# Optimization experiments

Measured on AMD Instinct MI355X. Metric: run time of the kernel, lower is better.

The kernel has to match this reference:

```python
import jax, jax.numpy as jnp
import numpy as np

B, T, C, H = 2, 2048, 1024, 16
HD = C // H
MAX_WAVELENGTH = 10000.0


def apply_rope(x, positions):
    # x: [B, H, T, HD], positions: [T]
    fraction = 2.0 * jnp.arange(HD // 2, dtype=jnp.float32) / HD
    timescale = MAX_WAVELENGTH ** fraction  # [HD//2]
    sinusoid = positions[:, None] / timescale[None, :]  # [T, HD//2]
    sin = jnp.sin(sinusoid)
    cos = jnp.cos(sinusoid)
    first, second = jnp.split(x, 2, axis=-1)
    out = jnp.concatenate(
        [first * cos - second * sin, second * cos + first * sin], axis=-1
    )
    return out.astype(x.dtype)


def setup_inputs() -> dict:
    key = jax.random.key(0)
    k1, k2, k3 = jax.random.split(key, 3)
    x = jax.random.normal(k1, (B, T, C), dtype=jnp.float32)
    w_attn = jax.random.normal(k2, (C, 3 * C), dtype=jnp.float32) * 0.02
    b_attn = jnp.zeros((3 * C,), dtype=jnp.float32)
    w_proj = jax.random.normal(k3, (C, C), dtype=jnp.float32) * 0.02
    b_proj = jnp.zeros((C,), dtype=jnp.float32)
    return {"x": x, "w_attn": w_attn, "b_attn": b_attn,
            "w_proj": w_proj, "b_proj": b_proj}


def reference(x, w_attn, b_attn, w_proj, b_proj):
    b, t, c = x.shape
    qkv = x @ w_attn + b_attn  # [B, T, 3C]
    q, k, v = jnp.split(qkv, 3, axis=-1)
    q = q.reshape(b, t, H, HD).transpose(0, 2, 1, 3)  # [B, H, T, HD]
    k = k.reshape(b, t, H, HD).transpose(0, 2, 1, 3)
    v = v.reshape(b, t, H, HD).transpose(0, 2, 1, 3)
    positions = jnp.arange(t, dtype=x.dtype)
    q = apply_rope(q, positions)
    k = apply_rope(k, positions)
    att = jnp.einsum('bhqd,bhkd->bhqk', q, k) * (1.0 / jnp.sqrt(HD))
    causal = jnp.tril(jnp.ones((t, t), dtype=bool))
    att = jnp.where(causal, att, jnp.finfo(att.dtype).min)
    att = jax.nn.softmax(att, axis=-1)
    y = jnp.einsum('bhqk,bhkd->bhqd', att, v)
    y = y.transpose(0, 2, 1, 3).reshape(b, t, c)
    return y @ w_proj + b_proj
```

## Files before the change

### kernel.cpp

```cpp
#include <hip/hip_runtime.h>
#include <hip/hip_bf16.h>


typedef __attribute__((ext_vector_type(8))) short short8;
typedef __attribute__((ext_vector_type(4))) float floatx4;

__device__ __forceinline__ unsigned short f2bf(float f) {
    union { float f; unsigned int u; } v; v.f = f;
    unsigned int r = v.u + 0x7FFFu + ((v.u >> 16) & 1u);
    return (unsigned short)(r >> 16);
}

__device__ __forceinline__ unsigned int pk2bf(float a, float b) {
    union { float f; unsigned int u; } ua, ub;
    ua.f = a; ub.f = b;
    return __builtin_amdgcn_perm(ub.u + 0x8000u, ua.u + 0x8000u, 0x07060302u);
}

__device__ __forceinline__ void gld16(const void* g, void* l) {
    __builtin_amdgcn_global_load_lds(
        (const __attribute__((address_space(1))) unsigned int*)g,
        (__attribute__((address_space(3))) unsigned int*)l, 16, 0, 0);
}

__device__ __forceinline__ void transpose_body(
    const float* __restrict__ in, unsigned short* __restrict__ out,
    int R, int NC, int bx, int by, int tid,
    unsigned short (*tile)[65]) {
    int r0 = by * 64, c0 = bx * 64;
    int col = tid & 63, rr = tid >> 6;
#pragma unroll
    for (int i = 0; i < 16; i++) {
        int row = rr + i * 4;
        tile[row][col] = f2bf(in[(size_t)(r0 + row) * NC + c0 + col]);
    }
    __syncthreads();
#pragma unroll
    for (int i = 0; i < 16; i++) {
        int orow = rr + i * 4;
        out[(size_t)(c0 + orow) * R + r0 + col] = tile[col][orow];
    }
}

__global__ __launch_bounds__(256) void prep(
    const float* __restrict__ x,
    const float* __restrict__ w_attn,
    const float* __restrict__ w_proj,
    unsigned short* __restrict__ x_bf,
    unsigned short* __restrict__ wTa,
    unsigned short* __restrict__ wTp,
    float2* __restrict__ tab) {
    __shared__ unsigned short tile[64][65];
    int bid = blockIdx.x;
    int tid = threadIdx.x;
    if (bid < 4096) {
        int i = bid * 256 + tid;
        float4 v = ((const float4*)x)[i];
        ushort4 o;
        o.x = f2bf(v.x); o.y = f2bf(v.y); o.z = f2bf(v.z); o.w = f2bf(v.w);
        ((ushort4*)x_bf)[i] = o;
    } else if (bid < 4864) {
        int t = bid - 4096;
        transpose_body(w_attn, wTa, 1024, 3072, t % 48, t / 48, tid, tile);
    } else if (bid < 5120) {
        int t = bid - 4864;
        transpose_body(w_proj, wTp, 1024, 1024, t & 15, t >> 4, tid, tile);
    } else {
        int i = (bid - 5120) * 256 + tid;
        int t = i >> 5, d = i & 31;
        float inv_ts = exp2f(-0.41524101186092036f * (float)d);
        float ang = (float)t * inv_ts;
        tab[i] = make_float2(sinf(ang), cosf(ang));
    }
}

__global__ __launch_bounds__(256) void gemm_qkv(
    const unsigned short* __restrict__ A,
    const unsigned short* __restrict__ BT,
    const float* __restrict__ bias,
    const float2* __restrict__ tab,
    unsigned short* __restrict__ qT,
    unsigned short* __restrict__ kT,
    unsigned short* __restrict__ vT) {
    __shared__ __align__(16) unsigned short smem[16384];
    unsigned short* as = smem;
    unsigned short* bs = smem + 8192;
    int tid = threadIdx.x;
    int lane = tid & 63;
    int w = tid >> 6;
    int wx = w & 1, wy = w >> 1;
    int l16 = lane & 15, quad = lane >> 4;
    int m0 = blockIdx.y * 128;
    int n0 = blockIdx.x * 128;
    int x = l16 & 7;
    int lr = lane >> 3;
    int gc = (lane & 7) ^ lr;

    floatx4 acc[4][4];
#pragma unroll
    for (int mi = 0; mi < 4; mi++)
#pragma unroll
        for (int ni = 0; ni < 4; ni++)
            acc[mi][ni] = (floatx4){0.f, 0.f, 0.f, 0.f};

    for (int k0 = 0; k0 < 1024; k0 += 64) {
        __syncthreads();
#pragma unroll
        for (int i = 0; i < 4; i++) {
            int seg = w * 4 + i;
            int row = seg * 8 + lr;
            gld16(A + (size_t)(m0 + row) * 1024 + k0 + gc * 8, &as[seg * 512]);
            gld16(BT + (size_t)(n0 + row) * 1024 + k0 + gc * 8, &bs[seg * 512]);
        }
        __syncthreads();
#pragma unroll
        for (int kk = 0; kk < 2; kk++) {
            short8 af[4], bf[4];
#pragma unroll
            for (int mi = 0; mi < 4; mi++) {
                int r = wy * 64 + mi * 16 + l16;
                af[mi] = *(const short8*)&as[r * 64 + (((kk << 2) | quad) ^ x) * 8];
            }
#pragma unroll
            for (int ni = 0; ni < 4; ni++) {
                int r = wx * 64 + ni * 16 + l16;
                bf[ni] = *(const short8*)&bs[r * 64 + (((kk << 2) | quad) ^ x) * 8];
            }
#pragma unroll
            for (int mi = 0; mi < 4; mi++)
#pragma unroll
                for (int ni = 0; ni < 4; ni++)
                    acc[mi][ni] = __builtin_amdgcn_mfma_f32_16x16x32_bf16(
                        af[mi], bf[ni], acc[mi][ni], 0, 0, 0);
        }
    }

    int region = n0 >> 10;
    int b = m0 >> 11;
    float b0 = bias[n0 + wx * 64 + l16];
    float b1 = bias[n0 + wx * 64 + 16 + l16];
    float b2 = bias[n0 + wx * 64 + 32 + l16];
    float b3 = bias[n0 + wx * 64 + 48 + l16];

    if (region < 2) {
        unsigned short* qk = region ? kT : qT;
        float scale = region ? 1.0f : 0.125f;
        int h = ((n0 & 1023) + wx * 64) >> 6;
        unsigned short* obase = qk + (size_t)(b * 16 + h) * 2048 * 64;
#pragma unroll
        for (int mi = 0; mi < 4; mi++)
#pragma unroll
            for (int r = 0; r < 4; r++) {
                int t = (m0 & 2047) + wy * 64 + mi * 16 + quad * 4 + r;
                float2 sc0 = tab[t * 32 + l16];
                float2 sc1 = tab[t * 32 + 16 + l16];
                float v1 = acc[mi][0][r] + b0, v2 = acc[mi][2][r] + b2;
                float w1 = acc[mi][1][r] + b1, w2 = acc[mi][3][r] + b3;
                unsigned short* orow = obase + (size_t)t * 64;
                orow[l16]      = f2bf((v1 * sc0.y - v2 * sc0.x) * scale);
                orow[l16 + 32] = f2bf((v2 * sc0.y + v1 * sc0.x) * scale);
                orow[l16 + 16] = f2bf((w1 * sc1.y - w2 * sc1.x) * scale);
                orow[l16 + 48] = f2bf((w2 * sc1.y + w1 * sc1.x) * scale);
            }
    } else {
        __syncthreads();
#pragma unroll
        for (int mi = 0; mi < 4; mi++)
#pragma unroll
            for (int ni = 0; ni < 4; ni++) {
                int d_loc = wx * 64 + ni * 16 + l16;
                int t_base = wy * 64 + mi * 16 + quad * 4;
                float bv = (ni == 0) ? b0 : (ni == 1) ? b1 : (ni == 2) ? b2 : b3;
                uint2 pk;
                pk.x = pk2bf(acc[mi][ni][0] + bv, acc[mi][ni][1] + bv);
                pk.y = pk2bf(acc[mi][ni][2] + bv, acc[mi][ni][3] + bv);
                int e = d_loc * 128 + (t_base ^ ((d_loc & 15) << 3));
                *(uint2*)&smem[e] = pk;
            }
        __syncthreads();
        int d_r = tid >> 1, half = tid & 1;
        int cv = (n0 - 2048) + d_r;
        int hh = cv >> 6, dd = cv & 63;
        int fofs = (d_r & 15) << 3;
        size_t vbase = ((size_t)(b * 16 + hh) * 64 + dd) * 2048 + (m0 & 2047);
#pragma unroll
        for (int c = 0; c < 8; c++) {
            int tc = half * 64 + c * 8;
            short8 val = *(const short8*)&smem[d_r * 128 + (tc ^ fofs)];
            *(short8*)&vT[vbase + tc] = val;
        }
    }
}

__global__ __launch_bounds__(256) void gemm_proj(
    const unsigned short* __restrict__ A,
    const unsigned short* __restrict__ BT,
    const float* __restrict__ bias,
    float* __restrict__ out) {
    __shared__ __align__(16) unsigned short as[128 * 64];
    __shared__ __align__(16) unsigned short bs[64 * 64];
    int lane = threadIdx.x & 63;
    int w = threadIdx.x >> 6;
    int wx = w & 1, wy = w >> 1;
    int l16 = lane & 15, quad = lane >> 4;
    int m0 = blockIdx.y * 128;
    int n0 = blockIdx.x * 64;
    int x = l16 & 7;
    int lr = lane >> 3;
    int gc = (lane & 7) ^ lr;

    floatx4 acc[4][2];
#pragma unroll
    for (int mi = 0; mi < 4; mi++)
#pragma unroll
        for (int ni = 0; ni < 2; ni++)
            acc[mi][ni] = (floatx4){0.f, 0.f, 0.f, 0.f};

    for (int k0 = 0; k0 < 1024; k0 += 64) {
        __syncthreads();
#pragma unroll
        for (int i = 0; i < 6; i++) {
            int seg = w * 6 + i;
            if (seg < 16) {
                int row = seg * 8 + lr;
                gld16(A + (size_t)(m0 + row) * 1024 + k0 + gc * 8, &as[seg * 512]);
            } else {
                int s2 = seg - 16;
                int row = s2 * 8 + lr;
                gld16(BT + (size_t)(n0 + row) * 1024 + k0 + gc * 8, &bs[s2 * 512]);
            }
        }
        __syncthreads();
#pragma unroll
        for (int kk = 0; kk < 2; kk++) {
            short8 af[4], bf[2];
#pragma unroll
            for (int mi = 0; mi < 4; mi++) {
                int r = wy * 64 + mi * 16 + l16;
                af[mi] = *(const short8*)&as[r * 64 + (((kk << 2) | quad) ^ x) * 8];
            }
#pragma unroll
            for (int ni = 0; ni < 2; ni++) {
                int r = wx * 32 + ni * 16 + l16;
                bf[ni] = *(const short8*)&bs[r * 64 + (((kk << 2) | quad) ^ x) * 8];
            }
#pragma unroll
            for (int mi = 0; mi < 4; mi++)
#pragma unroll
                for (int ni = 0; ni < 2; ni++)
                    acc[mi][ni] = __builtin_amdgcn_mfma_f32_16x16x32_bf16(
                        af[mi], bf[ni], acc[mi][ni], 0, 0, 0);
        }
    }

#pragma unroll
    for (int mi = 0; mi < 4; mi++)
#pragma unroll
        for (int ni = 0; ni < 2; ni++) {
            int row = m0 + wy * 64 + mi * 16 + quad * 4;
            int col = n0 + wx * 32 + ni * 16 + l16;
            float bv = bias[col];
#pragma unroll
            for (int r = 0; r < 4; r++)
                out[(size_t)(row + r) * 1024 + col] = acc[mi][ni][r] + bv;
        }
}

__global__ __launch_bounds__(512) void attn4(
    const unsigned short* __restrict__ qT,
    const unsigned short* __restrict__ kT,
    const unsigned short* __restrict__ vT,
    unsigned short* __restrict__ y) {
    __shared__ __align__(16) unsigned short kbuf[2][64 * 64];
    __shared__ __align__(16) unsigned short vbuf[2][64 * 64];
    __shared__ __align__(16) unsigned short pl[8][16 * 88];
    int lane = threadIdx.x & 63;
    int w = threadIdx.x >> 6;
    int l16 = lane & 15, quad = lane >> 4;
    int blk = blockIdx.x;
    int idx = blk >> 5;
    int qb = (idx < 8) ? (15 - idx * 2) : ((idx - 8) * 2);
    int bh = blk & 31;
    int b = bh >> 4, h = bh & 15;
    int q0 = qb * 128 + w * 16;
    int dt = 2 * qb + (w >> 2);
    const unsigned short* qp = qT + (size_t)bh * 2048 * 64;
    const unsigned short* kp = kT + (size_t)bh * 2048 * 64;
    const unsigned short* vp = vT + (size_t)bh * 64 * 2048;
    unsigned short* plw = pl[w];
    int x = l16 & 7;

    short8 qf0 = *(const short8*)(qp + (size_t)(q0 + l16) * 64 + quad * 8);
    short8 qf1 = *(const short8*)(qp + (size_t)(q0 + l16) * 64 + 32 + quad * 8);

    floatx4 acc[4];
#pragma unroll
    for (int ni = 0; ni < 4; ni++) acc[ni] = (floatx4){0.f, 0.f, 0.f, 0.f};
    float l_part = 0.f;

    auto stage = [&](int bi, int j0) {
#pragma unroll
        for (int i = 0; i < 2; i++) {
            int t = w * 2 + i;
            if (t < 8) {
                int r = t * 8 + (lane >> 3);
                int c = (lane & 7) ^ (r & 7);
                gld16(kp + (size_t)(j0 + r) * 64 + c * 8, &kbuf[bi][t * 512]);
            } else {
                int s = t - 8;
                int d = s * 8 + (lane >> 3);
                int c = (lane & 7) ^ (d & 7);
                gld16(vp + (size_t)d * 2048 + j0 + c * 8, &vbuf[bi][s * 512]);
            }
        }
    };

    int L = 2 * qb + 2;
    stage(0, 0);
    for (int it = 0; it < L; it++) {
        int j0 = it * 64;
        int bi = it & 1;
        __syncthreads();
        if (it + 1 < L) stage(bi ^ 1, j0 + 64);
        if (it > dt) continue;
        const unsigned short* kb = kbuf[bi];
        const unsigned short* vb = vbuf[bi];
        bool diag = (it == dt);
        floatx4 s[4];
#pragma unroll
        for (int c = 0; c < 4; c++) {
            int r = c * 16 + l16;
            short8 kf0 = *(const short8*)&kb[r * 64 + ((quad) ^ x) * 8];
            short8 kf1 = *(const short8*)&kb[r * 64 + ((quad | 4) ^ x) * 8];
            floatx4 z = (floatx4){0.f, 0.f, 0.f, 0.f};
            z = __builtin_amdgcn_mfma_f32_16x16x32_bf16(kf0, qf0, z, 0, 0, 0);
            z = __builtin_amdgcn_mfma_f32_16x16x32_bf16(kf1, qf1, z, 0, 0, 0);
            s[c] = z;
        }
        int query = q0 + l16;
#pragma unroll
        for (int c = 0; c < 4; c++) {
            float p[4];
#pragma unroll
            for (int r = 0; r < 4; r++) {
                float e = __expf(s[c][r]);
                if (diag) {
                    int key = j0 + c * 16 + quad * 4 + r;
                    e = (key <= query) ? e : 0.f;
                }
                p[r] = e;
            }
            l_part += (p[0] + p[1]) + (p[2] + p[3]);
            uint2 pk = {pk2bf(p[0], p[1]), pk2bf(p[2], p[3])};
            *(uint2*)&plw[l16 * 88 + c * 16 + quad * 4] = pk;
        }
        short8 pa0 = *(const short8*)&plw[l16 * 88 + quad * 8];
        short8 pa1 = *(const short8*)&plw[l16 * 88 + 32 + quad * 8];
#pragma unroll
        for (int ni = 0; ni < 4; ni++) {
            int d = ni * 16 + l16;
            short8 vf0 = *(const short8*)&vb[d * 64 + ((quad) ^ x) * 8];
            short8 vf1 = *(const short8*)&vb[d * 64 + ((quad | 4) ^ x) * 8];
            acc[ni] = __builtin_amdgcn_mfma_f32_16x16x32_bf16(pa0, vf0, acc[ni], 0, 0, 0);
            acc[ni] = __builtin_amdgcn_mfma_f32_16x16x32_bf16(pa1, vf1, acc[ni], 0, 0, 0);
        }
    }

    float tot = l_part;
    tot += __shfl_xor(tot, 16, 64);
    tot += __shfl_xor(tot, 32, 64);
    float inv[4];
#pragma unroll
    for (int r = 0; r < 4; r++)
        inv[r] = 1.f / __shfl(tot, quad * 4 + r, 16);
#pragma unroll
    for (int ni = 0; ni < 4; ni++)
#pragma unroll
        for (int r = 0; r < 4; r++) {
            int t = q0 + quad * 4 + r;
            y[((size_t)(b * 2048 + t)) * 1024 + h * 64 + ni * 16 + l16] =
                f2bf(acc[ni][r] * inv[r]);
        }
}

extern "C" void kernel_launch(void* const* d_in, const int* in_sizes, int n_in,
                              void* d_out, int out_size, void* d_ws, size_t ws_size,
                              hipStream_t stream) {
    const float* x      = (const float*)d_in[0];
    const float* w_attn = (const float*)d_in[1];
    const float* b_attn = (const float*)d_in[2];
    const float* w_proj = (const float*)d_in[3];
    const float* b_proj = (const float*)d_in[4];
    float* out = (float*)d_out;

    char* ws = (char*)d_ws;
    unsigned short* x_bf = (unsigned short*)ws;
    unsigned short* wTa  = (unsigned short*)(ws + (8ull << 20));
    unsigned short* wTp  = (unsigned short*)(ws + (14ull << 20));
    unsigned short* qTb  = (unsigned short*)(ws + (16ull << 20));
    unsigned short* kTb  = (unsigned short*)(ws + (24ull << 20));
    unsigned short* vTb  = (unsigned short*)(ws + (32ull << 20));
    float2*         tab  = (float2*)(ws + (40ull << 20));
    unsigned short* y_bf = x_bf;

    prep<<<5376, 256, 0, stream>>>(x, w_attn, w_proj, x_bf, wTa, wTp, tab);
    gemm_qkv<<<dim3(24, 32), 256, 0, stream>>>(x_bf, wTa, b_attn, tab,
                                               qTb, kTb, vTb);
    attn4<<<512, 512, 0, stream>>>(qTb, kTb, vTb, y_bf);
    gemm_proj<<<dim3(16, 32), 256, 0, stream>>>(y_bf, wTp, b_proj, out);
}
```

Measured before the change: 182.7 us.

## Give each attention wave two 16-row query tiles to reuse K/V fragments

The attention kernel now runs 4 waves per block instead of 8, and each wave handles 32 query rows as two 16-row tiles. Each K and V fragment read from LDS feeds two MFMAs, which halves LDS fragment traffic per query. Each wave now also stages four K/V chunks instead of two. The cost is higher register use from doubled accumulators, and fewer waves available to hide latency.

```diff
diff --git a/kernel.cpp b/kernel.cpp
--- a/kernel.cpp
+++ b/kernel.cpp
@@ -266,14 +266,14 @@
         }
 }
 
-__global__ __launch_bounds__(512) void attn4(
+__global__ __launch_bounds__(256) void attn5(
     const unsigned short* __restrict__ qT,
     const unsigned short* __restrict__ kT,
     const unsigned short* __restrict__ vT,
     unsigned short* __restrict__ y) {
     __shared__ __align__(16) unsigned short kbuf[2][64 * 64];
     __shared__ __align__(16) unsigned short vbuf[2][64 * 64];
-    __shared__ __align__(16) unsigned short pl[8][16 * 88];
+    __shared__ __align__(16) unsigned short pl[4][32 * 88];
     int lane = threadIdx.x & 63;
     int w = threadIdx.x >> 6;
     int l16 = lane & 15, quad = lane >> 4;
@@ -282,26 +282,31 @@
     int qb = (idx < 8) ? (15 - idx * 2) : ((idx - 8) * 2);
     int bh = blk & 31;
     int b = bh >> 4, h = bh & 15;
-    int q0 = qb * 128 + w * 16;
-    int dt = 2 * qb + (w >> 2);
+    int q0 = qb * 128 + w * 32;
+    int dt = 2 * qb + (w >> 1);
     const unsigned short* qp = qT + (size_t)bh * 2048 * 64;
     const unsigned short* kp = kT + (size_t)bh * 2048 * 64;
     const unsigned short* vp = vT + (size_t)bh * 64 * 2048;
     unsigned short* plw = pl[w];
     int x = l16 & 7;
 
-    short8 qf0 = *(const short8*)(qp + (size_t)(q0 + l16) * 64 + quad * 8);
-    short8 qf1 = *(const short8*)(qp + (size_t)(q0 + l16) * 64 + 32 + quad * 8);
-
-    floatx4 acc[4];
-#pragma unroll
-    for (int ni = 0; ni < 4; ni++) acc[ni] = (floatx4){0.f, 0.f, 0.f, 0.f};
-    float l_part = 0.f;
+    short8 qA0 = *(const short8*)(qp + (size_t)(q0 + l16) * 64 + quad * 8);
+    short8 qA1 = *(const short8*)(qp + (size_t)(q0 + l16) * 64 + 32 + quad * 8);
+    short8 qB0 = *(const short8*)(qp + (size_t)(q0 + 16 + l16) * 64 + quad * 8);
+    short8 qB1 = *(const short8*)(qp + (size_t)(q0 + 16 + l16) * 64 + 32 + quad * 8);
+
+    floatx4 accA[4], accB[4];
+#pragma unroll
+    for (int ni = 0; ni < 4; ni++) {
+        accA[ni] = (floatx4){0.f, 0.f, 0.f, 0.f};
+        accB[ni] = (floatx4){0.f, 0.f, 0.f, 0.f};
+    }
+    float lpA = 0.f, lpB = 0.f;
 
     auto stage = [&](int bi, int j0) {
 #pragma unroll
-        for (int i = 0; i < 2; i++) {
-            int t = w * 2 + i;
+        for (int i = 0; i < 4; i++) {
+            int t = w * 4 + i;
             if (t < 8) {
                 int r = t * 8 + (lane >> 3);
                 int c = (lane & 7) ^ (r & 7);
@@ -326,60 +331,74 @@
         const unsigned short* kb = kbuf[bi];
         const unsigned short* vb = vbuf[bi];
         bool diag = (it == dt);
-        floatx4 s[4];
+        int queryA = q0 + l16, queryB = q0 + 16 + l16;
 #pragma unroll
         for (int c = 0; c < 4; c++) {
             int r = c * 16 + l16;
             short8 kf0 = *(const short8*)&kb[r * 64 + ((quad) ^ x) * 8];
             short8 kf1 = *(const short8*)&kb[r * 64 + ((quad | 4) ^ x) * 8];
-            floatx4 z = (floatx4){0.f, 0.f, 0.f, 0.f};
-            z = __builtin_amdgcn_mfma_f32_16x16x32_bf16(kf0, qf0, z, 0, 0, 0);
-            z = __builtin_amdgcn_mfma_f32_16x16x32_bf16(kf1, qf1, z, 0, 0, 0);
-            s[c] = z;
-        }
-        int query = q0 + l16;
-#pragma unroll
-        for (int c = 0; c < 4; c++) {
-            float p[4];
-#pragma unroll
-            for (int r = 0; r < 4; r++) {
-                float e = __expf(s[c][r]);
+            floatx4 zA = (floatx4){0.f, 0.f, 0.f, 0.f};
+            zA = __builtin_amdgcn_mfma_f32_16x16x32_bf16(kf0, qA0, zA, 0, 0, 0);
+            zA = __builtin_amdgcn_mfma_f32_16x16x32_bf16(kf1, qA1, zA, 0, 0, 0);
+            floatx4 zB = (floatx4){0.f, 0.f, 0.f, 0.f};
+            zB = __builtin_amdgcn_mfma_f32_16x16x32_bf16(kf0, qB0, zB, 0, 0, 0);
+            zB = __builtin_amdgcn_mfma_f32_16x16x32_bf16(kf1, qB1, zB, 0, 0, 0);
+            float pA[4], pB[4];
+#pragma unroll
+            for (int rr = 0; rr < 4; rr++) {
+                float eA = __expf(zA[rr]);
+                float eB = __expf(zB[rr]);
                 if (diag) {
-                    int key = j0 + c * 16 + quad * 4 + r;
-                    e = (key <= query) ? e : 0.f;
+                    int key = j0 + c * 16 + quad * 4 + rr;
+                    eA = (key <= queryA) ? eA : 0.f;
+                    eB = (key <= queryB) ? eB : 0.f;
                 }
-                p[r] = e;
-            }
-            l_part += (p[0] + p[1]) + (p[2] + p[3]);
-            uint2 pk = {pk2bf(p[0], p[1]), pk2bf(p[2], p[3])};
-            *(uint2*)&plw[l16 * 88 + c * 16 + quad * 4] = pk;
-        }
-        short8 pa0 = *(const short8*)&plw[l16 * 88 + quad * 8];
-        short8 pa1 = *(const short8*)&plw[l16 * 88 + 32 + quad * 8];
+                pA[rr] = eA; pB[rr] = eB;
+            }
+            lpA += (pA[0] + pA[1]) + (pA[2] + pA[3]);
+            lpB += (pB[0] + pB[1]) + (pB[2] + pB[3]);
+            uint2 ka = {pk2bf(pA[0], pA[1]), pk2bf(pA[2], pA[3])};
+            uint2 kbv = {pk2bf(pB[0], pB[1]), pk2bf(pB[2], pB[3])};
+            *(uint2*)&plw[l16 * 88 + c * 16 + quad * 4] = ka;
+            *(uint2*)&plw[(16 + l16) * 88 + c * 16 + quad * 4] = kbv;
+        }
+        short8 paA0 = *(const short8*)&plw[l16 * 88 + quad * 8];
+        short8 paA1 = *(const short8*)&plw[l16 * 88 + 32 + quad * 8];
+        short8 paB0 = *(const short8*)&plw[(16 + l16) * 88 + quad * 8];
+        short8 paB1 = *(const short8*)&plw[(16 + l16) * 88 + 32 + quad * 8];
 #pragma unroll
         for (int ni = 0; ni < 4; ni++) {
             int d = ni * 16 + l16;
             short8 vf0 = *(const short8*)&vb[d * 64 + ((quad) ^ x) * 8];
             short8 vf1 = *(const short8*)&vb[d * 64 + ((quad | 4) ^ x) * 8];
-            acc[ni] = __builtin_amdgcn_mfma_f32_16x16x32_bf16(pa0, vf0, acc[ni], 0, 0, 0);
-            acc[ni] = __builtin_amdgcn_mfma_f32_16x16x32_bf16(pa1, vf1, acc[ni], 0, 0, 0);
-        }
-    }
-
-    float tot = l_part;
-    tot += __shfl_xor(tot, 16, 64);
-    tot += __shfl_xor(tot, 32, 64);
-    float inv[4];
-#pragma unroll
-    for (int r = 0; r < 4; r++)
-        inv[r] = 1.f / __shfl(tot, quad * 4 + r, 16);
+            accA[ni] = __builtin_amdgcn_mfma_f32_16x16x32_bf16(paA0, vf0, accA[ni], 0, 0, 0);
+            accA[ni] = __builtin_amdgcn_mfma_f32_16x16x32_bf16(paA1, vf1, accA[ni], 0, 0, 0);
+            accB[ni] = __builtin_amdgcn_mfma_f32_16x16x32_bf16(paB0, vf0, accB[ni], 0, 0, 0);
+            accB[ni] = __builtin_amdgcn_mfma_f32_16x16x32_bf16(paB1, vf1, accB[ni], 0, 0, 0);
+        }
+    }
+
+    float totA = lpA, totB = lpB;
+    totA += __shfl_xor(totA, 16, 64);
+    totA += __shfl_xor(totA, 32, 64);
+    totB += __shfl_xor(totB, 16, 64);
+    totB += __shfl_xor(totB, 32, 64);
+    float invA[4], invB[4];
+#pragma unroll
+    for (int r = 0; r < 4; r++) {
+        invA[r] = 1.f / __shfl(totA, quad * 4 + r, 16);
+        invB[r] = 1.f / __shfl(totB, quad * 4 + r, 16);
+    }
 #pragma unroll
     for (int ni = 0; ni < 4; ni++)
 #pragma unroll
         for (int r = 0; r < 4; r++) {
-            int t = q0 + quad * 4 + r;
-            y[((size_t)(b * 2048 + t)) * 1024 + h * 64 + ni * 16 + l16] =
-                f2bf(acc[ni][r] * inv[r]);
+            int tA = q0 + quad * 4 + r;
+            int tB = q0 + 16 + quad * 4 + r;
+            y[((size_t)(b * 2048 + tA)) * 1024 + h * 64 + ni * 16 + l16] =
+                f2bf(accA[ni][r] * invA[r]);
+            y[((size_t)(b * 2048 + tB)) * 1024 + h * 64 + ni * 16 + l16] =
+                f2bf(accB[ni][r] * invB[r]);
         }
 }
 
@@ -406,6 +425,6 @@
     prep<<<5376, 256, 0, stream>>>(x, w_attn, w_proj, x_bf, wTa, wTp, tab);
     gemm_qkv<<<dim3(24, 32), 256, 0, stream>>>(x_bf, wTa, b_attn, tab,
                                                qTb, kTb, vTb);
-    attn4<<<512, 512, 0, stream>>>(qTb, kTb, vTb, y_bf);
+    attn5<<<512, 256, 0, stream>>>(qTb, kTb, vTb, y_bf);
     gemm_proj<<<dim3(16, 32), 256, 0, stream>>>(y_bf, wTp, b_proj, out);
 }
```

New measurement: 202.3 us. +10.7%, slower.
